# Kernel tuning notes

Measured on AMD Instinct MI355X. Metric: run time of the kernel, lower is better.

Reference implementation:

```python
import jax, jax.numpy as jnp
import numpy as np

N_Q = 8        # out_channels = number of qubits
K = 4          # kernel_size
N_LAYERS = 2
STRIDE = 1
PAD = 1

def _c(x):
    return x.astype(jnp.complex64)

def _rx(t):
    c = _c(jnp.cos(t / 2)); s = _c(jnp.sin(t / 2))
    return jnp.stack([jnp.stack([c, -1j * s]), jnp.stack([-1j * s, c])])

def _ry(t):
    c = _c(jnp.cos(t / 2)); s = _c(jnp.sin(t / 2))
    return jnp.stack([jnp.stack([c, -s]), jnp.stack([s, c])])

def _rz(t):
    em = jnp.exp(-0.5j * t).astype(jnp.complex64)
    ep = jnp.exp(0.5j * t).astype(jnp.complex64)
    z = jnp.zeros((), jnp.complex64)
    return jnp.stack([jnp.stack([em, z]), jnp.stack([z, ep])])

def _apply1(psi, U, w):
    # apply 2x2 gate U on qubit w of statevector psi with shape (2,)*N_Q
    psi = jnp.moveaxis(psi, w, 0)
    sh = psi.shape
    psi = (U @ psi.reshape(2, -1)).reshape(sh)
    return jnp.moveaxis(psi, 0, w)

def _cnot(psi, c, t):
    psi = jnp.moveaxis(psi, (c, t), (0, 1))
    sh = psi.shape
    p = psi.reshape(2, 2, -1)
    p = jnp.stack([p[0], p[1, ::-1]], 0).reshape(sh)
    return jnp.moveaxis(p, (0, 1), (c, t))

def _ansatz(psi, wl):
    # custom_ansatz: per wire j -> RX, CNOT, RY, CNOT, RZ with ring entanglement
    for j in range(N_Q):
        c, t = (j, j + 1) if j < N_Q - 1 else (0, j)
        psi = _apply1(psi, _rx(wl[j]), j)
        psi = _cnot(psi, c, t)
        psi = _apply1(psi, _ry(wl[j]), j)
        psi = _cnot(psi, c, t)
        psi = _apply1(psi, _rz(wl[j]), j)
    return psi

def _circuit(ang, w):
    # ang: (K,) data angles, w: (N_LAYERS+1, N_Q) ansatz weights
    psi = jnp.zeros((2,) * N_Q, jnp.complex64).at[(0,) * N_Q].set(1.0)
    psi = _ansatz(psi, w[0])
    for i in range(K):                      # no_reupload data encoding
        psi = _apply1(psi, _ry(ang[i]), i)
    for l in range(1, N_LAYERS + 1):
        psi = _ansatz(psi, w[l])
    probs = jnp.abs(psi) ** 2
    outs = []
    for j in range(N_Q):                    # <Z_j> expectation values
        p = jnp.moveaxis(probs, j, 0).reshape(2, -1)
        outs.append(p[0].sum() - p[1].sum())
    return jnp.stack(outs)

def _quanv(x, w):
    # x: (B, C, L) -> (B, N_Q, n_seg)
    B, C, L = x.shape
    xp = jnp.pad(x, ((0, 0), (0, 0), (PAD, PAD)))
    n_seg = (L + 2 * PAD - K) // STRIDE + 1
    idx = jnp.arange(n_seg)[:, None] * STRIDE + jnp.arange(K)  # (n_seg, K)
    ang = xp[:, 0, :][:, idx]               # channel-0 windows as angles: (B, n_seg, K)
    out = jax.vmap(lambda a: _circuit(a, w))(ang.reshape(-1, K))  # (B*n_seg, N_Q)
    return out.reshape(B, n_seg, N_Q).transpose(0, 2, 1)

def setup_inputs() -> dict:
    key = jax.random.key(0)
    k0, k1, k2 = jax.random.split(key, 3)
    B, L = 32, 1024
    l1 = L + 2 * PAD - K + 1        # 1023
    l2 = l1 + 2 * PAD - K + 1       # 1022
    x = jax.random.normal(k0, (B, L, 1), jnp.float32)
    weights = jax.random.normal(k1, (N_LAYERS + 1, N_Q), jnp.float32)
    dense_w = jax.random.normal(k2, (l2, 1), jnp.float32) * 0.03
    dense_b = jnp.zeros((1,), jnp.float32)
    return {"x": x, "weights": weights, "dense_w": dense_w, "dense_b": dense_b}

def reference(x, weights, dense_w, dense_b):
    # weights are modded into [0, 2pi) in setup() and stop_gradient'ed in forward
    w = jax.lax.stop_gradient(jnp.mod(weights, 2 * jnp.pi))
    h = x.reshape(x.shape[0], x.shape[2], x.shape[1])   # (B, 1, L)
    h = jax.nn.relu(_quanv(h, w))                       # (B, N_Q, l1)
    h = jax.nn.relu(_quanv(h, w))                       # (B, N_Q, l2)
    pooled = h.max(axis=1)                              # channel max-pool -> (B, l2)
    return pooled @ dense_w + dense_b                   # Dense(1) -> (B, 1)
```

## Files before the change

kernel.cpp:

```cpp
#include <hip/hip_runtime.h>
#include <math.h>

#define TWO_PI 6.2831853071795864769f



__device__ __forceinline__ float2 shflx2(float2 a, int m) {
    return make_float2(__shfl_xor(a.x, m), __shfl_xor(a.y, m));
}

__device__ __forceinline__ void fused4(float2 v[4], int lane, int pcb, int ptb,
                                       float a2, float bb, float d2) {
    int M = pcb | ptb;
    int l1 = pcb >> 2, r1 = pcb & 3;
    int l2 = M >> 2,   r2 = M & 3;
    int l3 = ptb >> 2, r3 = ptb & 3;
    float2 o1[4], o2[4], o3[4];
#pragma unroll
    for (int r = 0; r < 4; ++r) {
        float2 s1 = v[r ^ r1]; o1[r] = l1 ? shflx2(s1, l1) : s1;
        float2 s2 = v[r ^ r2]; o2[r] = l2 ? shflx2(s2, l2) : s2;
        float2 s3 = v[r ^ r3]; o3[r] = l3 ? shflx2(s3, l3) : s3;
    }
#pragma unroll
    for (int r = 0; r < 4; ++r) {
        int k = (lane << 2) | r;
        float sA = (k & pcb) ? 1.f : -1.f;
        float bs = bb * sA, ds = d2 * sA;
        float nx = fmaf(a2, v[r].x, fmaf(bb, o1[r].y, fmaf(bs, o2[r].x,  ds * o3[r].y)));
        float ny = fmaf(a2, v[r].y, fmaf(-bb, o1[r].x, fmaf(bs, o2[r].y, -ds * o3[r].x)));
        v[r] = make_float2(nx, ny);
    }
}

__device__ __forceinline__ void wire7(float2 v[4], int lane, float a2, float bb, float d2) {
    float2 o[4];
#pragma unroll
    for (int r = 0; r < 4; ++r) o[r] = v[r ^ 1];
#pragma unroll
    for (int r = 0; r < 4; ++r) {
        int k = (lane << 2) | r;
        float s7 = (((k >> 7) ^ k) & 1) ? 1.f : -1.f;
        float Ax = a2, Ay = -d2 * s7, Bx = bb * s7, By = -bb;
        float nx = fmaf(Ax, v[r].x, fmaf(-Ay, v[r].y, fmaf(Bx, o[r].x, -By * o[r].y)));
        float ny = fmaf(Ax, v[r].y, fmaf( Ay, v[r].x, fmaf(Bx, o[r].y,  By * o[r].x)));
        v[r] = make_float2(nx, ny);
    }
}

__device__ __forceinline__ void rz2(float2 v[4], float2 u[4], int lane, int p,
                                    float ch, float sh) {
#pragma unroll
    for (int r = 0; r < 4; ++r) {
        int k = (lane << 2) | r;
        float s = ((k >> p) & 1) ? sh : -sh;
        v[r] = make_float2(fmaf(ch, v[r].x, -s * v[r].y),
                           fmaf(ch, v[r].y, s * v[r].x));
        u[r] = make_float2(fmaf(ch, u[r].x, -s * u[r].y),
                           fmaf(ch, u[r].y, s * u[r].x));
    }
}

__device__ __forceinline__ void ansatz2(float2 v[4], float2 u[4],
                                        const float* chs, const float* shs, int lane) {
#pragma unroll
    for (int j = 0; j < 7; ++j) {
        float ch = chs[j], sh = shs[j];
        float a2 = ch * ch, bb = ch * sh, d2 = sh * sh;
        int pcb = 1 << (7 - j), ptb = 1 << (6 - j);
        fused4(v, lane, pcb, ptb, a2, bb, d2);
        fused4(u, lane, pcb, ptb, a2, bb, d2);
        rz2(v, u, lane, 7 - j, ch, sh);
    }
    {
        float ch = chs[7], sh = shs[7];
        float a2 = ch * ch, bb = ch * sh, d2 = sh * sh;
        wire7(v, lane, a2, bb, d2);
        wire7(u, lane, a2, bb, d2);
        rz2(v, u, lane, 0, ch, sh);
    }
}

__device__ __forceinline__ void applyB(float2 v[4], int S, int lane) {
    int sbits = ((S & 1) << 7) | ((S & 2) << 5) | ((S & 4) << 3) | ((S & 8) << 1);
    int m = sbits >> 2;
    float2 nv[4];
#pragma unroll
    for (int r = 0; r < 4; ++r) {
        float2 o = shflx2(v[r], m);
        int k = (lane << 2) | r;
        float sg = (__popc(sbits & ~k) & 1) ? -1.f : 1.f;
        nv[r] = make_float2(sg * o.x, sg * o.y);
    }
#pragma unroll
    for (int r = 0; r < 4; ++r) v[r] = nv[r];
}

__global__ __launch_bounds__(64) void k_simh(const float* wt, float* H) {
    __shared__ float chs[24], shs[24];
    int lane = threadIdx.x;
    if (lane < 24) {
        float th = wt[lane];
        th = th - floorf(th / TWO_PI) * TWO_PI;
        float s, c;
        sincosf(0.5f * th, &s, &c);
        chs[lane] = c; shs[lane] = s;
    }
    __syncthreads();

    int i = blockIdx.x >> 4, j = blockIdx.x & 15;
    float2 v[4], u[4];
#pragma unroll
    for (int r = 0; r < 4; ++r) {
        v[r] = make_float2(0.f, 0.f);
        u[r] = make_float2(0.f, 0.f);
    }
    if (lane == 0) { v[0] = make_float2(1.f, 0.f); u[0] = make_float2(1.f, 0.f); }

    ansatz2(v, u, chs, shs, lane);
    applyB(v, i, lane);
    applyB(u, j, lane);
    ansatz2(v, u, chs + 8, shs + 8, lane);
    ansatz2(v, u, chs + 16, shs + 16, lane);

    float acc[8] = {0.f, 0.f, 0.f, 0.f, 0.f, 0.f, 0.f, 0.f};
#pragma unroll
    for (int r = 0; r < 4; ++r) {
        int k = (lane << 2) | r;
        float p = v[r].x * u[r].x + v[r].y * u[r].y;
#pragma unroll
        for (int q = 0; q < 8; ++q)
            acc[q] += ((k >> (7 - q)) & 1) ? -p : p;
    }
#pragma unroll
    for (int q = 0; q < 8; ++q) {
#pragma unroll
        for (int off = 32; off >= 1; off >>= 1)
            acc[q] += __shfl_xor(acc[q], off);
    }
    if (lane == 0) {
#pragma unroll
        for (int q = 0; q < 8; ++q)
            H[q * 256 + i * 16 + j] = acc[q];
    }
}

__global__ __launch_bounds__(256) void k_g(const float* H, float* G) {
    __shared__ float Hs[2048];
    int tid = threadIdx.x;
#pragma unroll
    for (int r = 0; r < 8; ++r) Hs[r * 256 + tid] = H[r * 256 + tid];
    __syncthreads();
    for (int e = tid; e < 928; e += 256) {
        int q = e / 116, rem = e - q * 116;
        int u = rem >> 2, comp = rem & 3;
        float acc = 0.f;
        if (u < 27 && comp < 3) {
            int t = u + 27 * comp;
            int td_[4] = {t % 3, (t / 3) % 3, (t / 9) % 3, t / 27};
            for (int cb = 0; cb < 16; ++cb) {
                int i = 0, j = 0; float sgn = 1.f;
#pragma unroll
                for (int k = 0; k < 4; ++k) {
                    int bk = (cb >> k) & 1;
                    if (td_[k] == 2) { i |= bk << k; j |= (1 - bk) << k; }
                    else { i |= bk << k; j |= bk << k;
                           if (td_[k] == 1 && bk) sgn = -sgn; }
                }
                acc += sgn * Hs[q * 256 + i * 16 + j];
            }
            acc *= 0.0625f;
        }
        G[e] = acc;
    }
}

__device__ __forceinline__ float contract4(const float4* Tq,
        float c0, float s0, float c1, float s1,
        float c2, float s2, float c3, float s3) {
    float l3[27];
#pragma unroll
    for (int u = 0; u < 27; ++u) {
        float4 g = Tq[u];
        l3[u] = fmaf(g.z, s3, fmaf(g.y, c3, g.x));
    }
    float l2[9];
#pragma unroll
    for (int u = 0; u < 9; ++u)
        l2[u] = fmaf(l3[u + 18], s2, fmaf(l3[u + 9], c2, l3[u]));
    float l1[3];
#pragma unroll
    for (int u = 0; u < 3; ++u)
        l1[u] = fmaf(l2[u + 6], s1, fmaf(l2[u + 3], c1, l2[u]));
    return fmaf(l1[2], s0, fmaf(l1[1], c0, l1[0]));
}

__global__ __launch_bounds__(256) void k_l1l2(const float* x, const float* G,
                                              const float* dw, float* partials) {
    __shared__ __align__(16) float Gs[928];
    __shared__ float xc[38], xs[38];
    __shared__ float yc[35], ysn[35];
    int tid = threadIdx.x;
    for (int e = tid; e < 928; e += 256) Gs[e] = G[e];

    int b = blockIdx.x >> 5;
    int c = blockIdx.x & 31;
    int base = c * 32 - 1;

    if (tid < 38) {
        int l = base - 1 + tid;
        float a = (l >= 0 && l < 1024) ? x[b * 1024 + l] : 0.f;
        sincosf(a, &xs[tid], &xc[tid]);
    }
    __syncthreads();

    if (tid < 35) {
        int s = base + tid;
        float y = 0.f;
        if (s >= 0 && s < 1023) {
            y = contract4((const float4*)Gs, xc[tid], xs[tid], xc[tid + 1], xs[tid + 1],
                          xc[tid + 2], xs[tid + 2], xc[tid + 3], xs[tid + 3]);
            y = fmaxf(y, 0.f);
        }
        sincosf(y, &ysn[tid], &yc[tid]);
    }
    __syncthreads();

    int wi = tid >> 3;
    int q = tid & 7;
    int widx = c * 32 + wi;
    float yq = -1e30f;
    if (widx < 1022) {
        yq = contract4((const float4*)&Gs[q * 116],
                       yc[wi], ysn[wi], yc[wi + 1], ysn[wi + 1],
                       yc[wi + 2], ysn[wi + 2], yc[wi + 3], ysn[wi + 3]);
    }
    yq = fmaxf(yq, __shfl_xor(yq, 1));
    yq = fmaxf(yq, __shfl_xor(yq, 2));
    yq = fmaxf(yq, __shfl_xor(yq, 4));
    float contrib = (q == 0 && widx < 1022) ? fmaxf(yq, 0.f) * dw[widx] : 0.f;
#pragma unroll
    for (int off = 1; off <= 32; off <<= 1) contrib += __shfl_xor(contrib, off);
    __shared__ float red[4];
    if ((tid & 63) == 0) red[tid >> 6] = contrib;
    __syncthreads();
    if (tid == 0)
        partials[blockIdx.x] = red[0] + red[1] + red[2] + red[3];
}

__global__ __launch_bounds__(256) void k_out(const float* partials, const float* db,
                                             float* out) {
    int t = threadIdx.x;
    int b = t >> 3, g = t & 7;
    float4 p = ((const float4*)partials)[(b << 3) | g];
    float s = (p.x + p.y) + (p.z + p.w);
    s += __shfl_xor(s, 1);
    s += __shfl_xor(s, 2);
    s += __shfl_xor(s, 4);
    if (g == 0) out[b] = s + db[0];
}

extern "C" void kernel_launch(void* const* d_in, const int* in_sizes, int n_in,
                              void* d_out, int out_size, void* d_ws, size_t ws_size,
                              hipStream_t stream) {
    const float* x  = (const float*)d_in[0];
    const float* wt = (const float*)d_in[1];
    const float* dw = (const float*)d_in[2];
    const float* db = (const float*)d_in[3];
    float* H        = (float*)d_ws;
    float* G        = (float*)d_ws + 2048;
    float* partials = (float*)d_ws + 2976;
    float* out = (float*)d_out;

    hipLaunchKernelGGL(k_simh, dim3(256),  dim3(64),  0, stream, wt, H);
    hipLaunchKernelGGL(k_g,    dim3(1),    dim3(256), 0, stream, H, G);
    hipLaunchKernelGGL(k_l1l2, dim3(1024), dim3(256), 0, stream, x, G, dw, partials);
    hipLaunchKernelGGL(k_out,  dim3(1),    dim3(256), 0, stream, partials, db, out);
}
```

Measured before the change: 25.78 us.

## Fuse G-build, quanv layers and output reduction into one kernel with atomics

Drops the separate k_g and k_out launches. The G tensor is now rebuilt redundantly inside every block of a new k_main kernel. Each block covers 128 output positions, computing four windows per thread with register reuse of the loaded G rows, instead of 32 positions per block over 1024 blocks. Per-batch results are accumulated with atomicAdd into an output pre-initialised with the bias by k_simh. This cuts launch overhead and the G/partials round trips, at the cost of redundant G computation per block and higher register pressure.

```diff
diff --git a/kernel.cpp b/kernel.cpp
--- a/kernel.cpp
+++ b/kernel.cpp
@@ -96,7 +96,8 @@
     for (int r = 0; r < 4; ++r) v[r] = nv[r];
 }
 
-__global__ __launch_bounds__(64) void k_simh(const float* wt, float* H) {
+__global__ __launch_bounds__(64) void k_simh(const float* wt, float* H,
+                                             const float* db, float* out) {
     __shared__ float chs[24], shs[24];
     int lane = threadIdx.x;
     if (lane < 24) {
@@ -106,6 +107,7 @@
         sincosf(0.5f * th, &s, &c);
         chs[lane] = c; shs[lane] = s;
     }
+    if (blockIdx.x == 0 && lane < 32) out[lane] = db[0];
     __syncthreads();
 
     int i = blockIdx.x >> 4, j = blockIdx.x & 15;
@@ -145,19 +147,47 @@
     }
 }
 
-__global__ __launch_bounds__(256) void k_g(const float* H, float* G) {
-    __shared__ float Hs[2048];
+#define GSTRIDE 116
+
+__global__ __launch_bounds__(256, 1) void k_main(const float* x, const float* H,
+                                                 const float* dw, float* out) {
+    __shared__ __align__(16) float Hs[2048];
+    __shared__ __align__(16) float Gs[8 * GSTRIDE];
+    __shared__ float2 xcs[134];
+    __shared__ float2 ycs[131];
+    __shared__ float dwc[128];
+    __shared__ float red[4];
     int tid = threadIdx.x;
-#pragma unroll
-    for (int r = 0; r < 8; ++r) Hs[r * 256 + tid] = H[r * 256 + tid];
-    __syncthreads();
+    int b = blockIdx.x >> 3, seg = blockIdx.x & 7;
+    int W0 = seg << 7;
+
+    {
+        const float4* H4 = (const float4*)H;
+        float4* Hs4 = (float4*)Hs;
+        Hs4[tid] = H4[tid];
+        Hs4[tid + 256] = H4[tid + 256];
+    }
+    if (tid < 134) {
+        int l = W0 - 2 + tid;
+        float a = (l >= 0 && l < 1024) ? x[b * 1024 + l] : 0.f;
+        float s, c; sincosf(a, &s, &c);
+        xcs[tid] = make_float2(c, s);
+    }
+    if (tid >= 128) {
+        int wl = tid - 128;
+        int widx = W0 + wl;
+        dwc[wl] = (widx < 1022) ? dw[widx] : 0.f;
+    }
+    __syncthreads();
+
     for (int e = tid; e < 928; e += 256) {
-        int q = e / 116, rem = e - q * 116;
+        int q = e / GSTRIDE, rem = e - q * GSTRIDE;
         int u = rem >> 2, comp = rem & 3;
-        float acc = 0.f;
+        float val = 0.f;
         if (u < 27 && comp < 3) {
             int t = u + 27 * comp;
             int td_[4] = {t % 3, (t / 3) % 3, (t / 9) % 3, t / 27};
+            float acc = 0.f;
             for (int cb = 0; cb < 16; ++cb) {
                 int i = 0, j = 0; float sgn = 1.f;
 #pragma unroll
@@ -169,95 +199,83 @@
                 }
                 acc += sgn * Hs[q * 256 + i * 16 + j];
             }
-            acc *= 0.0625f;
+            val = acc * 0.0625f;
         }
-        G[e] = acc;
-    }
-}
-
-__device__ __forceinline__ float contract4(const float4* Tq,
-        float c0, float s0, float c1, float s1,
-        float c2, float s2, float c3, float s3) {
-    float l3[27];
+        Gs[e] = val;
+    }
+    __syncthreads();
+
+    if (tid < 131) {
+        int s = W0 - 1 + tid;
+        float y = 0.f;
+        if (s >= 0 && s < 1023) {
+            float2 f0 = xcs[tid], f1 = xcs[tid + 1], f2 = xcs[tid + 2], f3 = xcs[tid + 3];
+            const float4* T0 = (const float4*)Gs;
+            float l3[27];
+#pragma unroll
+            for (int u = 0; u < 27; ++u) {
+                float4 g = T0[u];
+                l3[u] = fmaf(g.z, f3.y, fmaf(g.y, f3.x, g.x));
+            }
+            float l2[9];
+#pragma unroll
+            for (int u = 0; u < 9; ++u)
+                l2[u] = fmaf(l3[u + 18], f2.y, fmaf(l3[u + 9], f2.x, l3[u]));
+            float l1[3];
+#pragma unroll
+            for (int u = 0; u < 3; ++u)
+                l1[u] = fmaf(l2[u + 6], f1.y, fmaf(l2[u + 3], f1.x, l2[u]));
+            y = fmaf(l1[2], f0.y, fmaf(l1[1], f0.x, l1[0]));
+            y = fmaxf(y, 0.f);
+        }
+        float s_, c_; sincosf(y, &s_, &c_);
+        ycs[tid] = make_float2(c_, s_);
+    }
+    __syncthreads();
+
+    int q = tid & 7, wbase = tid >> 3;
+    const float4* Tq = (const float4*)&Gs[q * GSTRIDE];
+    float2 F0[4], F1[4], F2[4], F3[4];
+#pragma unroll
+    for (int w4 = 0; w4 < 4; ++w4) {
+        int wl = wbase + 32 * w4;
+        F0[w4] = ycs[wl];     F1[w4] = ycs[wl + 1];
+        F2[w4] = ycs[wl + 2]; F3[w4] = ycs[wl + 3];
+    }
+    float l3[4][27];
 #pragma unroll
     for (int u = 0; u < 27; ++u) {
         float4 g = Tq[u];
-        l3[u] = fmaf(g.z, s3, fmaf(g.y, c3, g.x));
-    }
-    float l2[9];
-#pragma unroll
-    for (int u = 0; u < 9; ++u)
-        l2[u] = fmaf(l3[u + 18], s2, fmaf(l3[u + 9], c2, l3[u]));
-    float l1[3];
-#pragma unroll
-    for (int u = 0; u < 3; ++u)
-        l1[u] = fmaf(l2[u + 6], s1, fmaf(l2[u + 3], c1, l2[u]));
-    return fmaf(l1[2], s0, fmaf(l1[1], c0, l1[0]));
-}
-
-__global__ __launch_bounds__(256) void k_l1l2(const float* x, const float* G,
-                                              const float* dw, float* partials) {
-    __shared__ __align__(16) float Gs[928];
-    __shared__ float xc[38], xs[38];
-    __shared__ float yc[35], ysn[35];
-    int tid = threadIdx.x;
-    for (int e = tid; e < 928; e += 256) Gs[e] = G[e];
-
-    int b = blockIdx.x >> 5;
-    int c = blockIdx.x & 31;
-    int base = c * 32 - 1;
-
-    if (tid < 38) {
-        int l = base - 1 + tid;
-        float a = (l >= 0 && l < 1024) ? x[b * 1024 + l] : 0.f;
-        sincosf(a, &xs[tid], &xc[tid]);
-    }
-    __syncthreads();
-
-    if (tid < 35) {
-        int s = base + tid;
-        float y = 0.f;
-        if (s >= 0 && s < 1023) {
-            y = contract4((const float4*)Gs, xc[tid], xs[tid], xc[tid + 1], xs[tid + 1],
-                          xc[tid + 2], xs[tid + 2], xc[tid + 3], xs[tid + 3]);
-            y = fmaxf(y, 0.f);
+#pragma unroll
+        for (int w4 = 0; w4 < 4; ++w4)
+            l3[w4][u] = fmaf(g.z, F3[w4].y, fmaf(g.y, F3[w4].x, g.x));
+    }
+    float contrib = 0.f;
+#pragma unroll
+    for (int w4 = 0; w4 < 4; ++w4) {
+        float l2[9];
+#pragma unroll
+        for (int u = 0; u < 9; ++u)
+            l2[u] = fmaf(l3[w4][u + 18], F2[w4].y, fmaf(l3[w4][u + 9], F2[w4].x, l3[w4][u]));
+        float l1[3];
+#pragma unroll
+        for (int u = 0; u < 3; ++u)
+            l1[u] = fmaf(l2[u + 6], F1[w4].y, fmaf(l2[u + 3], F1[w4].x, l2[u]));
+        float yq = fmaf(l1[2], F0[w4].y, fmaf(l1[1], F0[w4].x, l1[0]));
+        yq = fmaxf(yq, __shfl_xor(yq, 1));
+        yq = fmaxf(yq, __shfl_xor(yq, 2));
+        yq = fmaxf(yq, __shfl_xor(yq, 4));
+        if (q == 0) {
+            int wl = wbase + 32 * w4;
+            contrib = fmaf(fmaxf(yq, 0.f), dwc[wl], contrib);
         }
-        sincosf(y, &ysn[tid], &yc[tid]);
-    }
-    __syncthreads();
-
-    int wi = tid >> 3;
-    int q = tid & 7;
-    int widx = c * 32 + wi;
-    float yq = -1e30f;
-    if (widx < 1022) {
-        yq = contract4((const float4*)&Gs[q * 116],
-                       yc[wi], ysn[wi], yc[wi + 1], ysn[wi + 1],
-                       yc[wi + 2], ysn[wi + 2], yc[wi + 3], ysn[wi + 3]);
-    }
-    yq = fmaxf(yq, __shfl_xor(yq, 1));
-    yq = fmaxf(yq, __shfl_xor(yq, 2));
-    yq = fmaxf(yq, __shfl_xor(yq, 4));
-    float contrib = (q == 0 && widx < 1022) ? fmaxf(yq, 0.f) * dw[widx] : 0.f;
+    }
 #pragma unroll
     for (int off = 1; off <= 32; off <<= 1) contrib += __shfl_xor(contrib, off);
-    __shared__ float red[4];
     if ((tid & 63) == 0) red[tid >> 6] = contrib;
     __syncthreads();
     if (tid == 0)
-        partials[blockIdx.x] = red[0] + red[1] + red[2] + red[3];
-}
-
-__global__ __launch_bounds__(256) void k_out(const float* partials, const float* db,
-                                             float* out) {
-    int t = threadIdx.x;
-    int b = t >> 3, g = t & 7;
-    float4 p = ((const float4*)partials)[(b << 3) | g];
-    float s = (p.x + p.y) + (p.z + p.w);
-    s += __shfl_xor(s, 1);
-    s += __shfl_xor(s, 2);
-    s += __shfl_xor(s, 4);
-    if (g == 0) out[b] = s + db[0];
+        atomicAdd(&out[b], (red[0] + red[1]) + (red[2] + red[3]));
 }
 
 extern "C" void kernel_launch(void* const* d_in, const int* in_sizes, int n_in,
@@ -267,13 +285,9 @@
     const float* wt = (const float*)d_in[1];
     const float* dw = (const float*)d_in[2];
     const float* db = (const float*)d_in[3];
-    float* H        = (float*)d_ws;
-    float* G        = (float*)d_ws + 2048;
-    float* partials = (float*)d_ws + 2976;
+    float* H   = (float*)d_ws;
     float* out = (float*)d_out;
 
-    hipLaunchKernelGGL(k_simh, dim3(256),  dim3(64),  0, stream, wt, H);
-    hipLaunchKernelGGL(k_g,    dim3(1),    dim3(256), 0, stream, H, G);
-    hipLaunchKernelGGL(k_l1l2, dim3(1024), dim3(256), 0, stream, x, G, dw, partials);
-    hipLaunchKernelGGL(k_out,  dim3(1),    dim3(256), 0, stream, partials, db, out);
-}
+    hipLaunchKernelGGL(k_simh, dim3(256), dim3(64),  0, stream, wt, H, db, out);
+    hipLaunchKernelGGL(k_main, dim3(256), dim3(256), 0, stream, x, H, dw, out);
+}
```

Measured after the change: 22.63 us. 12.2% less time.
